# Performance work log

Hardware: AMD Instinct MI355X
Metric: run time of the kernel (lower is better)

The kernel has to match this reference:

```python
import jax, jax.numpy as jnp
import numpy as np

N_NODES = 6000
DEG = 16
N_EDGES = N_NODES * DEG
D_MODEL = 256
D_MSG = 64
D_FF = 4 * D_MODEL
N_LAYERS = 3
N_SPECIES = 108
RBF_BINS = D_MODEL
RBF_VMIN, RBF_VMAX = 0.0, 8.0


def setup_inputs():
    key = jax.random.key(0)
    ks = jax.random.split(key, 16)
    rng = np.random.default_rng(0)
    # graph: each node i has DEG in-edges (dst block-structured), random sources
    atomic_number = jnp.asarray(rng.integers(1, N_SPECIES, N_NODES), dtype=jnp.int32)
    dst = np.repeat(np.arange(N_NODES), DEG)
    src = rng.integers(0, N_NODES, N_EDGES)
    # angle graph t: nodes = edges of g; edges = all ordered pairs of in-edges sharing dst
    pq = np.array([(p, q) for p in range(DEG) for q in range(DEG) if p != q], dtype=np.int64)
    off = (np.arange(N_NODES) * DEG)[:, None]
    t_src = (off + pq[:, 0][None, :]).reshape(-1)
    t_dst = (off + pq[:, 1][None, :]).reshape(-1)
    r = jax.random.normal(ks[0], (N_EDGES, 3), dtype=jnp.float32) * 2.0  # bond vectors, |r|~3A
    s_dm = 1.0 / np.sqrt(D_MODEL)
    s_dmsg = 1.0 / np.sqrt(D_MSG)
    s_ff = 1.0 / np.sqrt(D_FF)
    return {
        'r': r,
        'atomic_number': atomic_number,
        'src': jnp.asarray(src, dtype=jnp.int32),
        'dst': jnp.asarray(dst, dtype=jnp.int32),
        't_src': jnp.asarray(t_src, dtype=jnp.int32),
        't_dst': jnp.asarray(t_dst, dtype=jnp.int32),
        'emb': jax.random.normal(ks[1], (N_SPECIES, D_MODEL), dtype=jnp.float32),
        'Wsrc': jax.random.normal(ks[2], (N_LAYERS, D_MSG, D_MODEL), dtype=jnp.float32) * s_dm,
        'bsrc': jnp.zeros((N_LAYERS, D_MSG), jnp.float32),
        'Wdst': jax.random.normal(ks[3], (N_LAYERS, D_MSG, D_MODEL), dtype=jnp.float32) * s_dm,
        'bdst': jnp.zeros((N_LAYERS, D_MSG), jnp.float32),
        'Wedge': jax.random.normal(ks[4], (N_LAYERS, D_MSG, D_MODEL), dtype=jnp.float32) * s_dm,
        'bedge': jnp.zeros((N_LAYERS, D_MSG), jnp.float32),
        'attn': jax.random.normal(ks[5], (N_LAYERS, D_MSG), dtype=jnp.float32) * s_dmsg,
        'W1': jax.random.normal(ks[6], (N_LAYERS, D_FF, D_MSG), dtype=jnp.float32) * s_dmsg,
        'b1': jnp.zeros((N_LAYERS, D_FF), jnp.float32),
        'W2': jax.random.normal(ks[7], (N_LAYERS, D_MODEL, D_FF), dtype=jnp.float32) * s_ff,
        'b2': jnp.zeros((N_LAYERS, D_MODEL), jnp.float32),
        'Wfc': jax.random.normal(ks[8], (1, D_MODEL), dtype=jnp.float32) * s_dm,
        'bfc': jnp.zeros((1,), jnp.float32),
    }


def _segment_softmax(logits, seg, num):
    m = jax.ops.segment_max(logits, seg, num_segments=num)
    ex = jnp.exp(logits - m[seg])
    z = jax.ops.segment_sum(ex, seg, num_segments=num)
    return ex / z[seg]


def reference(r, atomic_number, src, dst, t_src, t_dst, emb, Wsrc, bsrc, Wdst, bdst,
              Wedge, bedge, attn, W1, b1, W2, b2, Wfc, bfc):
    x = emb[atomic_number]                                   # [N, d_model]
    d = jnp.linalg.norm(r, axis=1)                           # [E]
    centers = jnp.linspace(RBF_VMIN, RBF_VMAX, RBF_BINS, dtype=r.dtype)
    gamma = 1.0 / (centers[1] - centers[0])
    y = jnp.exp(-gamma * (d[:, None] - centers[None, :]) ** 2)  # [E, d_model]
    rhat = r / d[:, None]
    # cos angle between edge pairs (sign of -r cancels in u_dot_v)
    cos_jik = jnp.clip(jnp.sum(rhat[t_src] * rhat[t_dst], axis=1), -1.0 + 1e-6, 1.0 - 1e-6)
    nch = jnp.arange(D_MSG, dtype=r.dtype)
    z_jik = jnp.cos(nch[None, :] * jnp.arccos(cos_jik)[:, None])  # Chebyshev T_k(cos) [T, 64]
    for l in range(N_LAYERS):
        xj = x @ Wsrc[l].T + bsrc[l]                          # [N, 64]
        xi = x @ Wdst[l].T + bdst[l]
        xij = xj[src] + xi[dst] + (y @ Wedge[l].T + bedge[l])  # [E, 64]
        e_jik = jax.nn.silu(z_jik + xij[t_src] + xij[t_dst])   # [T, 64]
        logits = e_jik @ attn[l]                               # [T]
        a = _segment_softmax(logits, t_dst, N_EDGES)           # edge_softmax over angle graph
        ft = jax.ops.segment_sum(a[:, None] * xij[t_src], t_dst, num_segments=N_EDGES)  # [E, 64]
        xn = jax.ops.segment_sum(ft, dst, num_segments=N_NODES)  # scatter to nodes [N, 64]
        x = jax.nn.silu(xn @ W1[l].T + b1[l]) @ W2[l].T + b2[l]  # FFN -> [N, d_model]
    atomwise = x @ Wfc.T + bfc                                  # [N, 1]
    return jnp.squeeze(jnp.mean(atomwise, axis=0))              # AvgPooling (eV/atom)


if __name__ == '__main__':
    out = reference(**setup_inputs())
    print(out)
```

## Files before the change

kernel.cpp:

```cpp
#include <hip/hip_runtime.h>

#define N_NODES 6000
#define DEG_    16
#define N_EDGES (N_NODES*DEG_)
#define D_MODEL 256
#define D_MSG   64
#define D_FF    1024

typedef __bf16 bf16x8 __attribute__((ext_vector_type(8)));
typedef float floatx4 __attribute__((ext_vector_type(4)));

__device__ __forceinline__ float silu_f(float v) {
    return v * __builtin_amdgcn_rcpf(1.0f + __expf(-v));
}
__device__ __forceinline__ float b2f(unsigned short u) {
    union { unsigned int i; float f; } v; v.i = ((unsigned int)u) << 16; return v.f;
}
__device__ __forceinline__ unsigned short f2b(float f) {
    union { float f; unsigned int i; } v; v.f = f;
    unsigned int r = (v.i + 0x7FFFu + ((v.i >> 16) & 1u)) >> 16;
    return (unsigned short)r;
}

#define WSRC_OFF 0
#define WDST_OFF 49152
#define WCVT_TOTAL 98304
#define CVT4_BLOCKS (WCVT_TOTAL/4/256)
#define EMB4_BLOCKS (N_NODES*D_MODEL/4/256)
#define GEOM_BLOCKS (N_EDGES/256)
#define WPACKE_BLOCKS 24
#define WPACK1_BLOCKS 96
__global__ __launch_bounds__(256) void prep_kernel(
    const float* __restrict__ Wsrc, const float* __restrict__ Wdst,
    const float* __restrict__ Wedge, const float* __restrict__ W1,
    unsigned short* __restrict__ wbf_out,
    const int* __restrict__ an, const float* __restrict__ emb,
    unsigned short* __restrict__ x,
    const float* __restrict__ r, float* __restrict__ d, float* __restrict__ rhat,
    unsigned short* __restrict__ wedgep,
    unsigned short* __restrict__ w1p) {
    int b = blockIdx.x;
    int t = threadIdx.x;
    if (b < CVT4_BLOCKS) {
        int i = (b*256 + t) * 4;
        const float* sp = (i < WDST_OFF) ? (Wsrc + i) : (Wdst + (i - WDST_OFF));
        float4 v = *(const float4*)sp;
        *(ushort4*)(wbf_out + i) = make_ushort4(f2b(v.x), f2b(v.y), f2b(v.z), f2b(v.w));
    } else if (b < CVT4_BLOCKS + EMB4_BLOCKS) {
        int i4 = (b - CVT4_BLOCKS)*256 + t;
        int node = i4 >> 6, c4 = i4 & 63;
        float4 v = *(const float4*)(emb + (size_t)an[node]*D_MODEL + c4*4);
        *(ushort4*)(x + (size_t)node*D_MODEL + c4*4) =
            make_ushort4(f2b(v.x), f2b(v.y), f2b(v.z), f2b(v.w));
    } else if (b < CVT4_BLOCKS + EMB4_BLOCKS + GEOM_BLOCKS) {
        int e = (b - CVT4_BLOCKS - EMB4_BLOCKS)*256 + t;
        float xx = r[e*3+0], yy = r[e*3+1], zz = r[e*3+2];
        float n = sqrtf(xx*xx + yy*yy + zz*zz);
        d[e] = n;
        float inv = 1.0f / n;
        *(float4*)(rhat + (size_t)e*4) = make_float4(xx*inv, yy*inv, zz*inv, 0.f);
    } else if (b < CVT4_BLOCKS + EMB4_BLOCKS + GEOM_BLOCKS + WPACKE_BLOCKS) {
        int wb = b - (CVT4_BLOCKS + EMB4_BLOCKS + GEOM_BLOCKS);
        int i = wb*256 + t;
        int lane = i & 63, ks = (i >> 6) & 7, rem = i >> 9;
        int ns = rem % 3, w = rem / 3;
        int row = 48*w + ns*16 + (lane & 15);
        int col = ks*32 + (lane >> 4)*8;
        const float* sp = Wedge + (size_t)row*256 + col;
        float4 v0 = *(const float4*)sp;
        float4 v1 = *(const float4*)(sp + 4);
        unsigned short h[8] = { f2b(v0.x), f2b(v0.y), f2b(v0.z), f2b(v0.w),
                                f2b(v1.x), f2b(v1.y), f2b(v1.z), f2b(v1.w) };
        *(uint4*)(wedgep + (size_t)i*8) = *(uint4*)h;
    } else {
        int wb = b - (CVT4_BLOCKS + EMB4_BLOCKS + GEOM_BLOCKS + WPACKE_BLOCKS);
        int i2 = wb*256 + t;
        int lp = i2 >> 13;
        int e = i2 & 8191;
        int lane = e & 63, j = (e >> 6) & 1, wv = (e >> 7) & 3, f = e >> 9;
        int row = f*64 + wv*16 + (lane & 15);
        int col = j*32 + (lane >> 4)*8;
        const float* sp = W1 + (size_t)lp*65536 + (size_t)row*64 + col;
        float4 v0 = *(const float4*)sp;
        float4 v1 = *(const float4*)(sp + 4);
        unsigned short h[8] = { f2b(v0.x), f2b(v0.y), f2b(v0.z), f2b(v0.w),
                                f2b(v1.x), f2b(v1.y), f2b(v1.z), f2b(v1.w) };
        *(uint4*)(w1p + (size_t)i2*8) = *(uint4*)h;
    }
}

#define APITCH 40
#define MCP 72
__global__ __launch_bounds__(256) void eplg_kernel(
    const unsigned short* __restrict__ Bwp,
    const float* __restrict__ bias,
    const float* __restrict__ dvec,
    unsigned short* __restrict__ C,
    const unsigned short* __restrict__ A,
    const unsigned short* __restrict__ B1g,
    const unsigned short* __restrict__ B2g,
    const float* __restrict__ bias1,
    const float* __restrict__ bias2,
    unsigned short* __restrict__ Cg,
    const float* __restrict__ Wsrc, const float* __restrict__ Wdst,
    const float* __restrict__ W2, const float* __restrict__ b2,
    const float* __restrict__ Wfc, const float* __restrict__ bfc,
    unsigned short* __restrict__ wcomb,
    float* __restrict__ bcomb,
    float* __restrict__ wfc2,
    float* __restrict__ out) {
    __shared__ __align__(16) unsigned short sm[5120];
    const int t = threadIdx.x;
    const int w = t >> 6, lane = t & 63, lr = lane & 15, lq = lane >> 4;

    if (blockIdx.x < 188) {
        unsigned short* As = sm;
        unsigned short* Bs = sm + 2560;
        unsigned short* Cs = sm;
        const int bid2 = blockIdx.x;
        const int bx = bid2 & 1;
        const int m0 = (bid2 >> 1) * 64;
        const unsigned short* B = bx ? B2g : B1g;
        const float* biasl = bx ? bias2 : bias1;
        const int n0 = bx * 64;
        const int K = 256, M = N_NODES, lda = 256, ldb = 256, ldc = 128;

        const int arow = t >> 2, achk = t & 3;

        floatx4 acc[4] = {};
        uint4 pa, pb;
        {
            int gm = m0 + arow;
            pa = (gm < M) ? *(const uint4*)(A + (size_t)gm*lda + achk*8) : make_uint4(0,0,0,0);
        }
        pb = *(const uint4*)(B + (size_t)arow*ldb + achk*8);

        for (int k0 = 0; k0 < K; k0 += 32) {
            *(uint4*)(&As[arow*APITCH + achk*8]) = pa;
            *(uint4*)(&Bs[arow*APITCH + achk*8]) = pb;
            __syncthreads();
            if (k0 + 32 < K) {
                int kn = k0 + 32;
                int gm = m0 + arow;
                pa = (gm < M) ? *(const uint4*)(A + (size_t)gm*lda + kn + achk*8) : make_uint4(0,0,0,0);
                pb = *(const uint4*)(B + (size_t)arow*ldb + kn + achk*8);
            }
            bf16x8 af, bfr[4];
            af = *(const bf16x8*)(&As[(w*16 + lr)*APITCH + lq*8]);
            #pragma unroll
            for (int ns = 0; ns < 4; ++ns)
                bfr[ns] = *(const bf16x8*)(&Bs[(ns*16 + lr)*APITCH + lq*8]);
            #pragma unroll
            for (int ns = 0; ns < 4; ++ns)
                acc[ns] = __builtin_amdgcn_mfma_f32_16x16x32_bf16(af, bfr[ns], acc[ns], 0,0,0);
            __syncthreads();
        }
        #pragma unroll
        for (int ns = 0; ns < 4; ++ns) {
            int bc = ns*16 + lr;
            float bv = biasl[bc];
            #pragma unroll
            for (int rg = 0; rg < 4; ++rg) {
                int lrow = w*16 + lq*4 + rg;
                Cs[lrow*MCP + bc] = f2b(acc[ns][rg] + bv);
            }
        }
        __syncthreads();
        #pragma unroll
        for (int it = 0; it < 2; ++it) {
            int i = t + it*256;
            int row = i >> 3, c8 = i & 7;
            int gm = m0 + row;
            if (gm < M)
                *(uint4*)(Cg + (size_t)gm*ldc + n0 + c8*8) = *(const uint4*)(Cs + row*MCP + c8*8);
        }
        return;
    }
    if (blockIdx.x < 257) {
        int b = blockIdx.x - 188;
        if (b < 64) {
            int lp  = 1 + (b >> 5);
            int wb2 = b & 31;
            const float* W2f = W2 + (size_t)(lp-1)*262144;
            const float* wm[4];
            #pragma unroll
            for (int i = 0; i < 4; ++i) {
                int row = wb2*4 + i;
                wm[i] = (row < 64) ? (Wsrc + (size_t)lp*16384 + row*256)
                                   : (Wdst + (size_t)lp*16384 + (row-64)*256);
            }
            float acc[4][4] = {};
            int c0 = t*4;
            #pragma unroll 8
            for (int c = 0; c < 256; ++c) {
                float4 w2v = *(const float4*)(W2f + (size_t)c*1024 + c0);
                #pragma unroll
                for (int i = 0; i < 4; ++i) {
                    float wv2 = wm[i][c];
                    acc[i][0] = fmaf(wv2, w2v.x, acc[i][0]);
                    acc[i][1] = fmaf(wv2, w2v.y, acc[i][1]);
                    acc[i][2] = fmaf(wv2, w2v.z, acc[i][2]);
                    acc[i][3] = fmaf(wv2, w2v.w, acc[i][3]);
                }
            }
            int fc = t >> 4, j = (t >> 3) & 1, lq2 = (t >> 1) & 3, cpos = (t & 1) * 4;
            #pragma unroll
            for (int i = 0; i < 4; ++i) {
                int row = wb2*4 + i;
                int wv2 = row >> 5, ns = (row >> 4) & 1, lr2 = row & 15;
                *(ushort4*)(wcomb + (size_t)(lp-1)*131072
                            + (size_t)fc*8192 + wv2*2048 + ns*1024 + j*512 + (lq2*16+lr2)*8 + cpos) =
                    make_ushort4(f2b(acc[i][0]), f2b(acc[i][1]), f2b(acc[i][2]), f2b(acc[i][3]));
            }
        } else if (b < 68) {
            int c = (b - 64)*256 + t;
            const float* W2f = W2 + 2*262144;
            float a0 = 0.f, a1 = 0.f, a2 = 0.f, a3 = 0.f;
            #pragma unroll 4
            for (int k = 0; k < 256; k += 4) {
                a0 = fmaf(Wfc[k+0], W2f[(size_t)(k+0)*1024 + c], a0);
                a1 = fmaf(Wfc[k+1], W2f[(size_t)(k+1)*1024 + c], a1);
                a2 = fmaf(Wfc[k+2], W2f[(size_t)(k+2)*1024 + c], a2);
                a3 = fmaf(Wfc[k+3], W2f[(size_t)(k+3)*1024 + c], a3);
            }
            wfc2[c] = (a0 + a1) + (a2 + a3);
        } else {
            int lp = 1 + (t >> 7);
            int row = t & 127;
            const float* b2l = b2 + (lp-1)*256;
            const float* wmrow = (row < 64) ? (Wsrc + (size_t)lp*16384 + row*256)
                                            : (Wdst + (size_t)lp*16384 + (row-64)*256);
            float acc = 0.f;
            #pragma unroll 8
            for (int c = 0; c < 256; ++c) acc += wmrow[c] * b2l[c];
            acc += (row < 64) ? bias1[lp*64 + row] : bias2[lp*64 + (row-64)];
            bcomb[(lp-1)*128 + row] = acc;
            if (t == 0) {
                float bo = 0.f;
                const float* b23 = b2 + 2*256;
                #pragma unroll 8
                for (int c = 0; c < 256; ++c) bo += Wfc[c] * b23[c];
                out[0] = bo + bfc[0];
            }
        }
        return;
    }
    {
        const int m0 = (blockIdx.x - 257) * 128;
        const float gamma = 31.875f;
        const float step  = 8.0f / 255.0f;
        bf16x8 af[2][8];
        #pragma unroll
        for (int s = 0; s < 2; ++s) {
            float dv = dvec[m0 + s*64 + w*16 + lr];
            #pragma unroll
            for (int ks = 0; ks < 8; ++ks) {
                unsigned short h[8];
                int kb = ks*32 + lq*8;
                #pragma unroll
                for (int j = 0; j < 8; ++j) {
                    float tt2 = dv - (float)(kb+j)*step;
                    h[j] = f2b(__expf(-gamma*tt2*tt2));
                }
                af[s][ks] = *(bf16x8*)h;
            }
        }
        const unsigned short* Bl = Bwp + lane*8;
        for (int ct = 0; ct < 12; ++ct) {
            const unsigned short* Bb = Bl + (ct/3)*12288 + (ct%3)*4096;
            uint4 pb[8];
            #pragma unroll
            for (int ks = 0; ks < 8; ++ks)
                pb[ks] = *(const uint4*)(Bb + ks*512);
            floatx4 acc0 = {}, acc1 = {};
            #pragma unroll
            for (int ks = 0; ks < 8; ++ks) {
                acc0 = __builtin_amdgcn_mfma_f32_16x16x32_bf16(
                    af[0][ks], *(const bf16x8*)&pb[ks], acc0, 0, 0, 0);
                acc1 = __builtin_amdgcn_mfma_f32_16x16x32_bf16(
                    af[1][ks], *(const bf16x8*)&pb[ks], acc1, 0, 0, 0);
            }
            int bc = (ct/3)*48 + (ct%3)*16 + lr;
            float bv = bias[bc];
            #pragma unroll
            for (int rg = 0; rg < 4; ++rg) {
                int row = m0 + w*16 + lq*4 + rg;
                C[(size_t)row*192 + bc] = f2b(acc0[rg] + bv);
                C[(size_t)(row + 64)*192 + bc] = f2b(acc1[rg] + bv);
            }
        }
    }
}

#define HP 72
#define CP2 136
__global__ __launch_bounds__(256) void ffw_kernel(
    const unsigned short* __restrict__ XN,
    const unsigned short* __restrict__ W1p,
    const float* __restrict__ b1l,
    const unsigned short* __restrict__ WCp,
    const float* __restrict__ bcl,
    unsigned short* __restrict__ XO,
    int M) {
    __shared__ __align__(16) unsigned short s_h[16*HP];
    __shared__ __align__(16) unsigned short s_c[16*CP2];
    const int t = threadIdx.x;
    const int wv = t >> 6, lane = t & 63, lr = lane & 15, lq = lane >> 4;
    const int m0 = blockIdx.x * 16;

    int ga = m0 + lr;
    bool aok = ga < M;
    uint4 a0 = aok ? *(const uint4*)(XN + (size_t)ga*64 + lq*8) : make_uint4(0,0,0,0);
    uint4 a1 = aok ? *(const uint4*)(XN + (size_t)ga*64 + 32 + lq*8) : make_uint4(0,0,0,0);

    floatx4 acc2[2] = {};

    const unsigned short* W1b = W1p + (size_t)wv*1024 + lane*8;
    const unsigned short* WCb = WCp + (size_t)wv*2048 + lane*8;

    uint4 pb1[2], pb2[4];
    pb1[0] = *(const uint4*)(W1b);
    pb1[1] = *(const uint4*)(W1b + 512);
    pb2[0] = *(const uint4*)(WCb);
    pb2[1] = *(const uint4*)(WCb + 512);
    pb2[2] = *(const uint4*)(WCb + 1024);
    pb2[3] = *(const uint4*)(WCb + 1536);

    for (int f = 0; f < 16; ++f) {
        uint4 cb1_0 = pb1[0], cb1_1 = pb1[1];
        uint4 cb2_0 = pb2[0], cb2_1 = pb2[1], cb2_2 = pb2[2], cb2_3 = pb2[3];
        float bv1 = b1l[f*64 + wv*16 + lr];
        if (f < 15) {
            const unsigned short* n1 = W1b + (f+1)*4096;
            const unsigned short* n2 = WCb + (f+1)*8192;
            pb1[0] = *(const uint4*)(n1);
            pb1[1] = *(const uint4*)(n1 + 512);
            pb2[0] = *(const uint4*)(n2);
            pb2[1] = *(const uint4*)(n2 + 512);
            pb2[2] = *(const uint4*)(n2 + 1024);
            pb2[3] = *(const uint4*)(n2 + 1536);
        }
        floatx4 hacc = {};
        hacc = __builtin_amdgcn_mfma_f32_16x16x32_bf16(
            *(const bf16x8*)&a0, *(const bf16x8*)&cb1_0, hacc, 0,0,0);
        hacc = __builtin_amdgcn_mfma_f32_16x16x32_bf16(
            *(const bf16x8*)&a1, *(const bf16x8*)&cb1_1, hacc, 0,0,0);
        {
            int col = wv*16 + lr;
            #pragma unroll
            for (int rg = 0; rg < 4; ++rg) {
                int row = lq*4 + rg;
                s_h[row*HP + col] = f2b(silu_f(hacc[rg] + bv1));
            }
        }
        __syncthreads();
        bf16x8 ha0 = *(const bf16x8*)(&s_h[lr*HP + lq*8]);
        bf16x8 ha1 = *(const bf16x8*)(&s_h[lr*HP + 32 + lq*8]);
        acc2[0] = __builtin_amdgcn_mfma_f32_16x16x32_bf16(ha0, *(const bf16x8*)&cb2_0, acc2[0], 0,0,0);
        acc2[0] = __builtin_amdgcn_mfma_f32_16x16x32_bf16(ha1, *(const bf16x8*)&cb2_1, acc2[0], 0,0,0);
        acc2[1] = __builtin_amdgcn_mfma_f32_16x16x32_bf16(ha0, *(const bf16x8*)&cb2_2, acc2[1], 0,0,0);
        acc2[1] = __builtin_amdgcn_mfma_f32_16x16x32_bf16(ha1, *(const bf16x8*)&cb2_3, acc2[1], 0,0,0);
        __syncthreads();
    }

    #pragma unroll
    for (int ns = 0; ns < 2; ++ns) {
        int col = wv*32 + ns*16 + lr;
        float bv = bcl[col];
        #pragma unroll
        for (int rg = 0; rg < 4; ++rg) {
            int row = lq*4 + rg;
            s_c[row*CP2 + col] = f2b(acc2[ns][rg] + bv);
        }
    }
    __syncthreads();
    {
        int row = t >> 4, c8 = t & 15;
        int gm = m0 + row;
        if (gm < M)
            *(uint4*)(XO + (size_t)gm*128 + c8*8) = *(const uint4*)(s_c + row*CP2 + c8*8);
    }
}

__global__ __launch_bounds__(256) void ffa_kernel(
    const unsigned short* __restrict__ XN,
    const unsigned short* __restrict__ W1p,
    const float* __restrict__ b1l,
    const float* __restrict__ wfc2,
    float* __restrict__ out, int M) {
    __shared__ float red[256];
    const int t = threadIdx.x;
    const int wv = t >> 6, lane = t & 63, lr = lane & 15, lq = lane >> 4;
    const int m0 = blockIdx.x * 16;

    int ga = m0 + lr;
    bool aok = ga < M;
    uint4 a0 = aok ? *(const uint4*)(XN + (size_t)ga*64 + lq*8) : make_uint4(0,0,0,0);
    uint4 a1 = aok ? *(const uint4*)(XN + (size_t)ga*64 + 32 + lq*8) : make_uint4(0,0,0,0);

    const unsigned short* W1b = W1p + (size_t)wv*1024 + lane*8;
    uint4 pb0 = *(const uint4*)(W1b);
    uint4 pb1 = *(const uint4*)(W1b + 512);

    float partial = 0.f;
    for (int f = 0; f < 16; ++f) {
        uint4 c0 = pb0, c1 = pb1;
        if (f < 15) {
            pb0 = *(const uint4*)(W1b + (f+1)*4096);
            pb1 = *(const uint4*)(W1b + (f+1)*4096 + 512);
        }
        floatx4 hacc = {};
        hacc = __builtin_amdgcn_mfma_f32_16x16x32_bf16(
            *(const bf16x8*)&a0, *(const bf16x8*)&c0, hacc, 0,0,0);
        hacc = __builtin_amdgcn_mfma_f32_16x16x32_bf16(
            *(const bf16x8*)&a1, *(const bf16x8*)&c1, hacc, 0,0,0);
        float bv1 = b1l[f*64 + wv*16 + lr];
        float wvv = wfc2[f*64 + wv*16 + lr];
        #pragma unroll
        for (int rg = 0; rg < 4; ++rg) {
            int gm = m0 + lq*4 + rg;
            if (gm < M) partial += silu_f(hacc[rg] + bv1) * wvv;
        }
    }
    red[t] = partial;
    __syncthreads();
    for (int off = 128; off > 0; off >>= 1) {
        if (t < off) red[t] += red[t+off];
        __syncthreads();
    }
    if (t == 0) atomicAdd(out, red[0] * (1.0f/(float)N_NODES));
}

__global__ __launch_bounds__(256) void angle_kernel(
    const unsigned short* __restrict__ xjxi,
    const unsigned short* __restrict__ eproj,
    const float* __restrict__ rhat,
    const int*   __restrict__ src,
    const float* __restrict__ attn,
    unsigned short* __restrict__ xn) {
    __shared__ __align__(16) float s_xij[16][68];
    __shared__ float s_rhat[16][4];
    __shared__ float s_logit[16][17];
    __shared__ float s_a[16][17];
    __shared__ float s_w[16];
    const int tt = threadIdx.x;
    const int node = blockIdx.x;

    if (tt < 16) {
        float4 rv = *(const float4*)(rhat + (size_t)(node*DEG_ + tt)*4);
        s_rhat[tt][0] = rv.x; s_rhat[tt][1] = rv.y; s_rhat[tt][2] = rv.z; s_rhat[tt][3] = 0.f;
        s_logit[tt][tt] = -1e30f;
    }
    {
        int p = tt >> 4, c4 = tt & 15;
        int e = node*DEG_ + p;
        int se = src[e];
        ushort4 aj = *(const ushort4*)(xjxi + (size_t)se*128 + c4*4);
        ushort4 ai = *(const ushort4*)(xjxi + (size_t)node*128 + 64 + c4*4);
        ushort4 ae = *(const ushort4*)(eproj + (size_t)e*192 + c4*4);
        s_xij[p][c4*4+0] = b2f(aj.x) + b2f(ai.x) + b2f(ae.x);
        s_xij[p][c4*4+1] = b2f(aj.y) + b2f(ai.y) + b2f(ae.y);
        s_xij[p][c4*4+2] = b2f(aj.z) + b2f(ai.z) + b2f(ae.z);
        s_xij[p][c4*4+3] = b2f(aj.w) + b2f(ai.w) + b2f(ae.w);
    }
    __syncthreads();
    int pp = 0, qq = 0;
    float lg = 0.f;
    if (tt < 240) {
        int pair = tt >> 1, half = tt & 1;
        pp = (int)((1.0f + sqrtf(8.0f*(float)pair + 1.0f)) * 0.5f);
        qq = pair - ((pp*(pp-1)) >> 1);
        float c = s_rhat[pp][0]*s_rhat[qq][0] + s_rhat[pp][1]*s_rhat[qq][1]
                + s_rhat[pp][2]*s_rhat[qq][2];
        c = fminf(fmaxf(c, -0.999999f), 0.999999f);
        float c2 = 2.0f * c;
        float tk0, tk1;
        if (half) {
            float T2  = fmaf(c2, c, -1.0f);
            float T3  = fmaf(2.0f*T2,  c,   -c);
            float T4  = fmaf(2.0f*T2,  T2,  -1.0f);
            float T7  = fmaf(2.0f*T4,  T3,  -c);
            float T8  = fmaf(2.0f*T4,  T4,  -1.0f);
            float T15 = fmaf(2.0f*T8,  T7,  -c);
            float T16 = fmaf(2.0f*T8,  T8,  -1.0f);
            float T31 = fmaf(2.0f*T16, T15, -c);
            float T32 = fmaf(2.0f*T16, T16, -1.0f);
            float T33 = fmaf(2.0f*T32, c,   -T31);
            tk0 = T32; tk1 = T33;
        } else {
            tk0 = 1.0f; tk1 = c;
        }
        const float* xp = &s_xij[pp][0] + half*32;
        const float* xq = &s_xij[qq][0] + half*32;
        const float* at = attn + half*32;
        float acc = 0.f;
        #pragma unroll
        for (int k0 = 0; k0 < 32; k0 += 4) {
            float4 xp4 = *(const float4*)(xp + k0);
            float4 xq4 = *(const float4*)(xq + k0);
            float a0 = at[k0+0], a1 = at[k0+1], a2 = at[k0+2], a3 = at[k0+3];
            float v0 = tk0 + xp4.x + xq4.x;
            acc = fmaf(a0, silu_f(v0), acc);
            { float tn2 = c2*tk1 - tk0; tk0 = tk1; tk1 = tn2; }
            float v1 = tk0 + xp4.y + xq4.y;
            acc = fmaf(a1, silu_f(v1), acc);
            { float tn2 = c2*tk1 - tk0; tk0 = tk1; tk1 = tn2; }
            float v2 = tk0 + xp4.z + xq4.z;
            acc = fmaf(a2, silu_f(v2), acc);
            { float tn2 = c2*tk1 - tk0; tk0 = tk1; tk1 = tn2; }
            float v3 = tk0 + xp4.w + xq4.w;
            acc = fmaf(a3, silu_f(v3), acc);
            { float tn2 = c2*tk1 - tk0; tk0 = tk1; tk1 = tn2; }
        }
        lg = acc;
    }
    lg += __shfl_xor(lg, 1);
    if (tt < 240 && (tt & 1) == 0) {
        s_logit[pp][qq] = lg;
        s_logit[qq][pp] = lg;
    }
    __syncthreads();
    {
        int q = tt >> 4, p = tt & 15;
        float l = s_logit[p][q];
        float m = l;
        m = fmaxf(m, __shfl_xor(m, 1));
        m = fmaxf(m, __shfl_xor(m, 2));
        m = fmaxf(m, __shfl_xor(m, 4));
        m = fmaxf(m, __shfl_xor(m, 8));
        float e = __expf(l - m);
        float z = e;
        z += __shfl_xor(z, 1);
        z += __shfl_xor(z, 2);
        z += __shfl_xor(z, 4);
        z += __shfl_xor(z, 8);
        s_a[p][q] = e * __builtin_amdgcn_rcpf(z);
    }
    __syncthreads();
    {
        int p = tt >> 4, q = tt & 15;
        float a = s_a[p][q];
        a += __shfl_xor(a, 1);
        a += __shfl_xor(a, 2);
        a += __shfl_xor(a, 4);
        a += __shfl_xor(a, 8);
        if (q == 0) s_w[p] = a;
    }
    __syncthreads();
    if (tt < 64) {
        float acc = 0.f;
        #pragma unroll
        for (int p = 0; p < 16; ++p) acc += s_w[p] * s_xij[p][tt];
        xn[(size_t)node*64 + tt] = f2b(acc);
    }
}

extern "C" void kernel_launch(void* const* d_in, const int* in_sizes, int n_in,
                              void* d_out, int out_size, void* d_ws, size_t ws_size,
                              hipStream_t stream) {
    (void)in_sizes; (void)n_in; (void)out_size; (void)ws_size;
    const float* r    = (const float*)d_in[0];
    const int*   an   = (const int*)  d_in[1];
    const int*   src  = (const int*)  d_in[2];
    const float* emb  = (const float*)d_in[6];
    const float* Wsrc = (const float*)d_in[7];
    const float* bsrc = (const float*)d_in[8];
    const float* Wdst = (const float*)d_in[9];
    const float* bdst = (const float*)d_in[10];
    const float* Wedge= (const float*)d_in[11];
    const float* bedge= (const float*)d_in[12];
    const float* attn = (const float*)d_in[13];
    const float* W1   = (const float*)d_in[14];
    const float* b1   = (const float*)d_in[15];
    const float* W2   = (const float*)d_in[16];
    const float* b2   = (const float*)d_in[17];
    const float* Wfc  = (const float*)d_in[18];
    const float* bfc  = (const float*)d_in[19];

    char* ws = (char*)d_ws;
    float* d_d              = (float*)(ws);
    float* d_rhat           = (float*)(ws + 384000);
    unsigned short* wbf     = (unsigned short*)(ws + 1920000);
    unsigned short* d_x     = (unsigned short*)(ws + 4180992);
    unsigned short* d_xjxi  = (unsigned short*)(ws + 7252992);
    unsigned short* d_eproj = (unsigned short*)(ws + 8788992);
    unsigned short* d_xn    = (unsigned short*)(ws + 45652992);
    unsigned short* d_wcomb = (unsigned short*)(ws + 46420992);
    float* d_bcomb          = (float*)(ws + 46945280);
    float* d_wfc2           = (float*)(ws + 46946304);
    unsigned short* d_wedgep= (unsigned short*)(ws + 46950400);
    unsigned short* d_w1p   = (unsigned short*)(ws + 47048704);
    float* out = (float*)d_out;

    unsigned short* wsrc_bf  = wbf + WSRC_OFF;
    unsigned short* wdst_bf  = wbf + WDST_OFF;

    prep_kernel<<<CVT4_BLOCKS + EMB4_BLOCKS + GEOM_BLOCKS + WPACKE_BLOCKS + WPACK1_BLOCKS,
                  256, 0, stream>>>(
        Wsrc, Wdst, Wedge, W1, wbf, an, emb, d_x, r, d_d, d_rhat, d_wedgep, d_w1p);

    eplg_kernel<<<188 + 69 + 750, 256, 0, stream>>>(
        d_wedgep, bedge, d_d, d_eproj,
        d_x, wsrc_bf, wdst_bf, bsrc, bdst, d_xjxi,
        Wsrc, Wdst, W2, b2, Wfc, bfc,
        d_wcomb, d_bcomb, d_wfc2, out);

    angle_kernel<<<N_NODES, 256, 0, stream>>>(
        d_xjxi, d_eproj, d_rhat, src, attn, d_xn);
    ffw_kernel<<<375, 256, 0, stream>>>(
        d_xn, d_w1p, b1, d_wcomb, d_bcomb, d_xjxi, N_NODES);

    angle_kernel<<<N_NODES, 256, 0, stream>>>(
        d_xjxi, d_eproj + 64, d_rhat, src, attn + 64, d_xn);
    ffw_kernel<<<375, 256, 0, stream>>>(
        d_xn, d_w1p + 65536, b1 + 1024, d_wcomb + 131072, d_bcomb + 128, d_xjxi, N_NODES);

    angle_kernel<<<N_NODES, 256, 0, stream>>>(
        d_xjxi, d_eproj + 128, d_rhat, src, attn + 128, d_xn);
    ffa_kernel<<<375, 256, 0, stream>>>(
        d_xn, d_w1p + 131072, b1 + 2048, d_wfc2, out, N_NODES);
}
```

Baseline: 230.1 us.

## Replace per-edge RBF edge projection with interpolated distance lookup table

The per-edge Gaussian-RBF expansion followed by the bf16 MFMA projection through Wedge is replaced. A 1024-entry table over distance (0 to 9) is built in fp32 in the eplg kernel. The angle kernels then linearly interpolate that table by each edge's distance instead of reading a precomputed per-edge bf16 eproj buffer. This removes a large edge-level GEMM, the Wedge packing in prep, and the large eproj write and reads. In exchange it adds interpolation error, clamps distances beyond the table range, and adds a small table gather per edge.

```diff
diff --git a/kernel.cpp b/kernel.cpp
--- a/kernel.cpp
+++ b/kernel.cpp
@@ -7,6 +7,9 @@
 #define D_MSG   64
 #define D_FF    1024
 
+#define TBL_N   1024
+#define TBL_DMAX 9.0f
+
 typedef __bf16 bf16x8 __attribute__((ext_vector_type(8)));
 typedef float floatx4 __attribute__((ext_vector_type(4)));
 
@@ -28,16 +31,14 @@
 #define CVT4_BLOCKS (WCVT_TOTAL/4/256)
 #define EMB4_BLOCKS (N_NODES*D_MODEL/4/256)
 #define GEOM_BLOCKS (N_EDGES/256)
-#define WPACKE_BLOCKS 24
 #define WPACK1_BLOCKS 96
 __global__ __launch_bounds__(256) void prep_kernel(
     const float* __restrict__ Wsrc, const float* __restrict__ Wdst,
-    const float* __restrict__ Wedge, const float* __restrict__ W1,
+    const float* __restrict__ W1,
     unsigned short* __restrict__ wbf_out,
     const int* __restrict__ an, const float* __restrict__ emb,
     unsigned short* __restrict__ x,
     const float* __restrict__ r, float* __restrict__ d, float* __restrict__ rhat,
-    unsigned short* __restrict__ wedgep,
     unsigned short* __restrict__ w1p) {
     int b = blockIdx.x;
     int t = threadIdx.x;
@@ -59,21 +60,8 @@
         d[e] = n;
         float inv = 1.0f / n;
         *(float4*)(rhat + (size_t)e*4) = make_float4(xx*inv, yy*inv, zz*inv, 0.f);
-    } else if (b < CVT4_BLOCKS + EMB4_BLOCKS + GEOM_BLOCKS + WPACKE_BLOCKS) {
+    } else {
         int wb = b - (CVT4_BLOCKS + EMB4_BLOCKS + GEOM_BLOCKS);
-        int i = wb*256 + t;
-        int lane = i & 63, ks = (i >> 6) & 7, rem = i >> 9;
-        int ns = rem % 3, w = rem / 3;
-        int row = 48*w + ns*16 + (lane & 15);
-        int col = ks*32 + (lane >> 4)*8;
-        const float* sp = Wedge + (size_t)row*256 + col;
-        float4 v0 = *(const float4*)sp;
-        float4 v1 = *(const float4*)(sp + 4);
-        unsigned short h[8] = { f2b(v0.x), f2b(v0.y), f2b(v0.z), f2b(v0.w),
-                                f2b(v1.x), f2b(v1.y), f2b(v1.z), f2b(v1.w) };
-        *(uint4*)(wedgep + (size_t)i*8) = *(uint4*)h;
-    } else {
-        int wb = b - (CVT4_BLOCKS + EMB4_BLOCKS + GEOM_BLOCKS + WPACKE_BLOCKS);
         int i2 = wb*256 + t;
         int lp = i2 >> 13;
         int e = i2 & 8191;
@@ -92,10 +80,6 @@
 #define APITCH 40
 #define MCP 72
 __global__ __launch_bounds__(256) void eplg_kernel(
-    const unsigned short* __restrict__ Bwp,
-    const float* __restrict__ bias,
-    const float* __restrict__ dvec,
-    unsigned short* __restrict__ C,
     const unsigned short* __restrict__ A,
     const unsigned short* __restrict__ B1g,
     const unsigned short* __restrict__ B2g,
@@ -108,6 +92,9 @@
     unsigned short* __restrict__ wcomb,
     float* __restrict__ bcomb,
     float* __restrict__ wfc2,
+    const float* __restrict__ WedgeF,
+    const float* __restrict__ bedge,
+    float* __restrict__ T,
     float* __restrict__ out) {
     __shared__ __align__(16) unsigned short sm[5120];
     const int t = threadIdx.x;
@@ -246,48 +233,39 @@
         return;
     }
     {
-        const int m0 = (blockIdx.x - 257) * 128;
+        int b = blockIdx.x - 257;
+        float* s_rbf = (float*)sm;
+        const int rl = t >> 5;
+        const int row = b*8 + rl;
+        const int cg = t & 31;
         const float gamma = 31.875f;
         const float step  = 8.0f / 255.0f;
-        bf16x8 af[2][8];
+        const float step_t = TBL_DMAX / (float)(TBL_N - 1);
+        float dv = (float)row * step_t;
+        {
+            int k0 = cg*8;
+            #pragma unroll
+            for (int j = 0; j < 8; ++j) {
+                float x2 = dv - (float)(k0+j)*step;
+                s_rbf[rl*260 + k0 + j] = __expf(-gamma*x2*x2);
+            }
+        }
+        __syncthreads();
+        const float* rb = s_rbf + rl*260;
         #pragma unroll
-        for (int s = 0; s < 2; ++s) {
-            float dv = dvec[m0 + s*64 + w*16 + lr];
-            #pragma unroll
-            for (int ks = 0; ks < 8; ++ks) {
-                unsigned short h[8];
-                int kb = ks*32 + lq*8;
-                #pragma unroll
-                for (int j = 0; j < 8; ++j) {
-                    float tt2 = dv - (float)(kb+j)*step;
-                    h[j] = f2b(__expf(-gamma*tt2*tt2));
-                }
-                af[s][ks] = *(bf16x8*)h;
-            }
-        }
-        const unsigned short* Bl = Bwp + lane*8;
-        for (int ct = 0; ct < 12; ++ct) {
-            const unsigned short* Bb = Bl + (ct/3)*12288 + (ct%3)*4096;
-            uint4 pb[8];
-            #pragma unroll
-            for (int ks = 0; ks < 8; ++ks)
-                pb[ks] = *(const uint4*)(Bb + ks*512);
-            floatx4 acc0 = {}, acc1 = {};
-            #pragma unroll
-            for (int ks = 0; ks < 8; ++ks) {
-                acc0 = __builtin_amdgcn_mfma_f32_16x16x32_bf16(
-                    af[0][ks], *(const bf16x8*)&pb[ks], acc0, 0, 0, 0);
-                acc1 = __builtin_amdgcn_mfma_f32_16x16x32_bf16(
-                    af[1][ks], *(const bf16x8*)&pb[ks], acc1, 0, 0, 0);
-            }
-            int bc = (ct/3)*48 + (ct%3)*16 + lr;
-            float bv = bias[bc];
-            #pragma unroll
-            for (int rg = 0; rg < 4; ++rg) {
-                int row = m0 + w*16 + lq*4 + rg;
-                C[(size_t)row*192 + bc] = f2b(acc0[rg] + bv);
-                C[(size_t)(row + 64)*192 + bc] = f2b(acc1[rg] + bv);
-            }
+        for (int c = 0; c < 6; ++c) {
+            int col = cg*6 + c;
+            const float* wr = WedgeF + (size_t)col*256;
+            float a0 = 0.f, a1 = 0.f, a2 = 0.f, a3 = 0.f;
+            #pragma unroll 4
+            for (int k = 0; k < 256; k += 4) {
+                float4 wv = *(const float4*)(wr + k);
+                a0 = fmaf(rb[k+0], wv.x, a0);
+                a1 = fmaf(rb[k+1], wv.y, a1);
+                a2 = fmaf(rb[k+2], wv.z, a2);
+                a3 = fmaf(rb[k+3], wv.w, a3);
+            }
+            T[(size_t)row*192 + col] = bedge[col] + (a0 + a1) + (a2 + a3);
         }
     }
 }
@@ -433,7 +411,9 @@
 
 __global__ __launch_bounds__(256) void angle_kernel(
     const unsigned short* __restrict__ xjxi,
-    const unsigned short* __restrict__ eproj,
+    const float* __restrict__ T,
+    int lc0,
+    const float* __restrict__ dvec,
     const float* __restrict__ rhat,
     const int*   __restrict__ src,
     const float* __restrict__ attn,
@@ -457,11 +437,17 @@
         int se = src[e];
         ushort4 aj = *(const ushort4*)(xjxi + (size_t)se*128 + c4*4);
         ushort4 ai = *(const ushort4*)(xjxi + (size_t)node*128 + 64 + c4*4);
-        ushort4 ae = *(const ushort4*)(eproj + (size_t)e*192 + c4*4);
-        s_xij[p][c4*4+0] = b2f(aj.x) + b2f(ai.x) + b2f(ae.x);
-        s_xij[p][c4*4+1] = b2f(aj.y) + b2f(ai.y) + b2f(ae.y);
-        s_xij[p][c4*4+2] = b2f(aj.z) + b2f(ai.z) + b2f(ae.z);
-        s_xij[p][c4*4+3] = b2f(aj.w) + b2f(ai.w) + b2f(ae.w);
+        const float inv_step_t = (float)(TBL_N - 1) / TBL_DMAX;
+        float u = fminf(dvec[e] * inv_step_t, (float)(TBL_N - 2) + 0.999f);
+        int i0 = (int)u;
+        float fr = u - (float)i0;
+        const float* t0 = T + (size_t)i0*192 + lc0 + c4*4;
+        float4 v0 = *(const float4*)t0;
+        float4 v1 = *(const float4*)(t0 + 192);
+        s_xij[p][c4*4+0] = b2f(aj.x) + b2f(ai.x) + fmaf(fr, v1.x - v0.x, v0.x);
+        s_xij[p][c4*4+1] = b2f(aj.y) + b2f(ai.y) + fmaf(fr, v1.y - v0.y, v0.y);
+        s_xij[p][c4*4+2] = b2f(aj.z) + b2f(ai.z) + fmaf(fr, v1.z - v0.z, v0.z);
+        s_xij[p][c4*4+3] = b2f(aj.w) + b2f(ai.w) + fmaf(fr, v1.w - v0.w, v0.w);
     }
     __syncthreads();
     int pp = 0, qq = 0;
@@ -583,40 +569,39 @@
     unsigned short* wbf     = (unsigned short*)(ws + 1920000);
     unsigned short* d_x     = (unsigned short*)(ws + 4180992);
     unsigned short* d_xjxi  = (unsigned short*)(ws + 7252992);
-    unsigned short* d_eproj = (unsigned short*)(ws + 8788992);
+    float* d_table          = (float*)(ws + 8788992);
     unsigned short* d_xn    = (unsigned short*)(ws + 45652992);
     unsigned short* d_wcomb = (unsigned short*)(ws + 46420992);
     float* d_bcomb          = (float*)(ws + 46945280);
     float* d_wfc2           = (float*)(ws + 46946304);
-    unsigned short* d_wedgep= (unsigned short*)(ws + 46950400);
     unsigned short* d_w1p   = (unsigned short*)(ws + 47048704);
     float* out = (float*)d_out;
 
     unsigned short* wsrc_bf  = wbf + WSRC_OFF;
     unsigned short* wdst_bf  = wbf + WDST_OFF;
 
-    prep_kernel<<<CVT4_BLOCKS + EMB4_BLOCKS + GEOM_BLOCKS + WPACKE_BLOCKS + WPACK1_BLOCKS,
+    prep_kernel<<<CVT4_BLOCKS + EMB4_BLOCKS + GEOM_BLOCKS + WPACK1_BLOCKS,
                   256, 0, stream>>>(
-        Wsrc, Wdst, Wedge, W1, wbf, an, emb, d_x, r, d_d, d_rhat, d_wedgep, d_w1p);
-
-    eplg_kernel<<<188 + 69 + 750, 256, 0, stream>>>(
-        d_wedgep, bedge, d_d, d_eproj,
+        Wsrc, Wdst, W1, wbf, an, emb, d_x, r, d_d, d_rhat, d_w1p);
+
+    eplg_kernel<<<188 + 69 + 128, 256, 0, stream>>>(
         d_x, wsrc_bf, wdst_bf, bsrc, bdst, d_xjxi,
         Wsrc, Wdst, W2, b2, Wfc, bfc,
-        d_wcomb, d_bcomb, d_wfc2, out);
+        d_wcomb, d_bcomb, d_wfc2,
+        Wedge, bedge, d_table, out);
 
     angle_kernel<<<N_NODES, 256, 0, stream>>>(
-        d_xjxi, d_eproj, d_rhat, src, attn, d_xn);
+        d_xjxi, d_table, 0, d_d, d_rhat, src, attn, d_xn);
     ffw_kernel<<<375, 256, 0, stream>>>(
         d_xn, d_w1p, b1, d_wcomb, d_bcomb, d_xjxi, N_NODES);
 
     angle_kernel<<<N_NODES, 256, 0, stream>>>(
-        d_xjxi, d_eproj + 64, d_rhat, src, attn + 64, d_xn);
+        d_xjxi, d_table, 64, d_d, d_rhat, src, attn + 64, d_xn);
     ffw_kernel<<<375, 256, 0, stream>>>(
         d_xn, d_w1p + 65536, b1 + 1024, d_wcomb + 131072, d_bcomb + 128, d_xjxi, N_NODES);
 
     angle_kernel<<<N_NODES, 256, 0, stream>>>(
-        d_xjxi, d_eproj + 128, d_rhat, src, attn + 128, d_xn);
+        d_xjxi, d_table, 128, d_d, d_rhat, src, attn + 128, d_xn);
     ffa_kernel<<<375, 256, 0, stream>>>(
         d_xn, d_w1p + 131072, b1 + 2048, d_wfc2, out, N_NODES);
 }
```

After: 243.3 us. 1.06x slower.
